# Performance work log

Hardware: AMD Instinct MI355X
Metric: run time of the kernel (lower is better)

## Reference

```python
import jax, jax.numpy as jnp
import numpy as np

B, L, N, D = 4096, 50, 50, 128
STD = 0.1


def setup_inputs() -> dict:
    key = jax.random.key(0)
    ks = jax.random.split(key, 6)
    seq_idx = jax.random.randint(ks[0], (B, L), 0, N, dtype=jnp.int32)
    mask = jnp.ones((B, L), dtype=jnp.int32)
    node_vectors = jax.random.normal(ks[1], (B, N, D), dtype=jnp.float32)
    u = lambda k, shp: jax.random.uniform(k, shp, jnp.float32, -STD, STD)
    return {
        "sequence_of_indexes": seq_idx,
        "mask": mask,
        "node_vectors": node_vectors,
        "batch_size": B,
        "W_last": u(ks[2], (D, D)),      # dense_last_item kernel (no bias)
        "W_seq": u(ks[3], (D, D)),       # dense_sequence_items kernel
        "b_seq": jnp.zeros((D,), jnp.float32),  # dense_sequence_items bias
        "W_alpha": u(ks[4], (D, 1)),     # dense_alpha kernel (no bias)
    }


def reference(sequence_of_indexes, mask, node_vectors, batch_size,
              W_last, W_seq, b_seq, W_alpha):
    maskf = mask.astype(jnp.float32)                          # [B, L]
    seq_len = jnp.sum(maskf, axis=1).astype(jnp.int32)        # [B]
    rows = jnp.arange(batch_size)
    # last item index per session, then gather its node vector
    last_idx = sequence_of_indexes[rows, seq_len - 1]         # [B]
    v_n = node_vectors[rows, last_idx]                        # [B, D]
    # per-batch embedding lookup: node_vectors[b, seq_idx[b]]
    v_i = jnp.take_along_axis(node_vectors, sequence_of_indexes[..., None], axis=1)  # [B, L, D]
    vn_proj = (v_n @ W_last)[:, None, :]                      # [B, 1, D]
    vi_proj = v_i @ W_seq + b_seq                             # [B, L, D]
    alpha = jax.nn.sigmoid(vn_proj + vi_proj) @ W_alpha       # [B, L, 1]
    alpha = alpha * maskf[..., None]
    session_graph = jnp.sum(alpha * v_i, axis=1)              # [B, D]
    return v_n, session_graph
```

## Files before the change

kernel.cpp:

```cpp
#include <hip/hip_runtime.h>
#include <math.h>

#define BB 4096
#define LL 50
#define NN 50
#define DD 128
#define STR 136

typedef short bf16x8 __attribute__((ext_vector_type(8)));
typedef float f32x4  __attribute__((ext_vector_type(4)));

static __device__ inline unsigned short f32_to_bf16_rne(float f) {
    unsigned int u = __float_as_uint(f);
    u += 0x7FFFu + ((u >> 16) & 1u);
    return (unsigned short)(u >> 16);
}
static __device__ inline float bf16_to_f32(unsigned short h) {
    return __uint_as_float(((unsigned int)h) << 16);
}

__global__ void prep_w(const float* __restrict__ W_seq,
                       const float* __restrict__ W_last,
                       unsigned short* __restrict__ ws)
{
    int t = blockIdx.x * blockDim.x + threadIdx.x;
    int lane = t & 63;
    int nt   = (t >> 6) & 7;
    int kk   = t >> 9;
    const float* W = (kk < 4) ? W_seq : W_last;
    int kb = (kk & 3) * 32 + (lane >> 4) * 8;
    int n  = nt * 16 + (lane & 15);
    unsigned short* dst = ws + (size_t)t * 8;
    #pragma unroll
    for (int j = 0; j < 8; ++j)
        dst[j] = f32_to_bf16_rne(W[(kb + j) * DD + n]);
}

__global__ __launch_bounds__(256, 3) void sess_attn(
    const int*   __restrict__ seq_idx,
    const int*   __restrict__ mask,
    const float* __restrict__ nodes,
    const float* __restrict__ b_seq,
    const float* __restrict__ W_alpha,
    const unsigned short* __restrict__ wfrag,
    float*       __restrict__ out)
{
    const int b    = blockIdx.x;
    const int tid  = threadIdx.x;
    const int lane = tid & 63;
    const int wave = tid >> 6;
    const int col  = lane & 15;
    const int quad = lane >> 4;

    __shared__ __align__(16) unsigned short s_nbf[64][STR];
    __shared__ float s_alpha[64];
    __shared__ float s_cntf[64];
    __shared__ int   s_last;

    const float4* nb4 = (const float4*)(nodes + (size_t)b * (NN * DD));
    float4 v[7];
    #pragma unroll
    for (int j = 0; j < 6; ++j) v[j] = nb4[tid + j * 256];
    if (tid < 64) v[6] = nb4[tid + 1536];

    const bf16x8* wsf = (const bf16x8*)wfrag;
    bf16x8 bfS[8], bfL[8];
    #pragma unroll
    for (int kk = 0; kk < 4; ++kk)
        #pragma unroll
        for (int j = 0; j < 2; ++j) {
            bfS[kk * 2 + j] = wsf[(size_t)(((kk    ) * 8 + wave * 2 + j) * 64 + lane)];
            bfL[kk * 2 + j] = wsf[(size_t)(((kk + 4) * 8 + wave * 2 + j) * 64 + lane)];
        }

    int pm = 0, pi = 0;
    if (tid < 64) {
        pm = (tid < LL) ? mask[b * LL + tid]    : 0;
        pi = (tid < LL) ? seq_idx[b * LL + tid] : 0;
    }

    float bb_r[2], wa_r[2];
    #pragma unroll
    for (int j = 0; j < 2; ++j) {
        int n = (wave * 2 + j) * 16 + col;
        bb_r[j] = b_seq[n];
        wa_r[j] = W_alpha[n];
    }

    if (tid < 64) { s_alpha[tid] = 0.f; s_cntf[tid] = 0.f; }

    #pragma unroll
    for (int j = 0; j < 6; ++j) {
        int idx = tid + j * 256;
        int r = idx >> 5, c = (idx & 31) * 4;
        ushort4 h;
        h.x = f32_to_bf16_rne(v[j].x);
        h.y = f32_to_bf16_rne(v[j].y);
        h.z = f32_to_bf16_rne(v[j].z);
        h.w = f32_to_bf16_rne(v[j].w);
        *(ushort4*)&s_nbf[r][c] = h;
    }
    if (tid < 64) {
        int idx = tid + 1536;
        int r = idx >> 5, c = (idx & 31) * 4;
        ushort4 h;
        h.x = f32_to_bf16_rne(v[6].x);
        h.y = f32_to_bf16_rne(v[6].y);
        h.z = f32_to_bf16_rne(v[6].z);
        h.w = f32_to_bf16_rne(v[6].w);
        *(ushort4*)&s_nbf[r][c] = h;
    }

    if (tid < 64) {
        int mm = pm;
        mm += __shfl_xor(mm, 1);  mm += __shfl_xor(mm, 2);
        mm += __shfl_xor(mm, 4);  mm += __shfl_xor(mm, 8);
        mm += __shfl_xor(mm, 16); mm += __shfl_xor(mm, 32);
        int j = mm - 1;
        if (j < 0) j += LL;
        int li = __shfl(pi, j);
        if (tid == 0) s_last = li;
        if (tid < LL && pm) atomicAdd(&s_cntf[pi], (float)pm);
    }
    __syncthreads();

    const int last = s_last;

    if (tid < DD)
        out[(size_t)b * DD + tid] = nodes[(size_t)b * (NN * DD) + last * DD + tid];

    f32x4 acc[4][2];
    #pragma unroll
    for (int m = 0; m < 4; ++m)
        #pragma unroll
        for (int j = 0; j < 2; ++j)
            acc[m][j] = (f32x4){0.f, 0.f, 0.f, 0.f};
    f32x4 accV[2];
    #pragma unroll
    for (int j = 0; j < 2; ++j)
        accV[j] = (f32x4){bb_r[j], bb_r[j], bb_r[j], bb_r[j]};

    #pragma unroll
    for (int kk = 0; kk < 4; ++kk) {
        bf16x8 a[4];
        #pragma unroll
        for (int m = 0; m < 4; ++m)
            a[m] = *(const bf16x8*)&s_nbf[m * 16 + col][kk * 32 + quad * 8];
        bf16x8 av = *(const bf16x8*)&s_nbf[last][kk * 32 + quad * 8];
        #pragma unroll
        for (int j = 0; j < 2; ++j) {
            #pragma unroll
            for (int m = 0; m < 4; ++m)
                acc[m][j] = __builtin_amdgcn_mfma_f32_16x16x32_bf16(
                    a[m], bfS[kk * 2 + j], acc[m][j], 0, 0, 0);
            accV[j] = __builtin_amdgcn_mfma_f32_16x16x32_bf16(
                av, bfL[kk * 2 + j], accV[j], 0, 0, 0);
        }
    }

    #pragma unroll
    for (int m = 0; m < 4; ++m) {
        float pr[4] = {0.f, 0.f, 0.f, 0.f};
        #pragma unroll
        for (int j = 0; j < 2; ++j) {
            float wa = wa_r[j];
            #pragma unroll
            for (int r = 0; r < 4; ++r) {
                float x = acc[m][j][r] + accV[j][r];
                float sig = 1.f / (1.f + __expf(-x));
                pr[r] = fmaf(sig, wa, pr[r]);
            }
        }
        #pragma unroll
        for (int r = 0; r < 4; ++r) {
            float vv = pr[r];
            vv += __shfl_xor(vv, 1);
            vv += __shfl_xor(vv, 2);
            vv += __shfl_xor(vv, 4);
            vv += __shfl_xor(vv, 8);
            int row = m * 16 + quad * 4 + r;
            if (col == 0 && row < NN) atomicAdd(&s_alpha[row], vv);
        }
    }
    __syncthreads();

    if (tid < DD) {
        float acc2 = 0.f;
        #pragma unroll 10
        for (int n = 0; n < NN; ++n)
            acc2 = fmaf(s_cntf[n] * s_alpha[n], bf16_to_f32(s_nbf[n][tid]), acc2);
        out[(size_t)BB * DD + (size_t)b * DD + tid] = acc2;
    }
}

extern "C" void kernel_launch(void* const* d_in, const int* in_sizes, int n_in,
                              void* d_out, int out_size, void* d_ws, size_t ws_size,
                              hipStream_t stream) {
    const int*   seq     = (const int*)  d_in[0];
    const int*   mask    = (const int*)  d_in[1];
    const float* nodes   = (const float*)d_in[2];
    const float* W_last  = (const float*)d_in[4];
    const float* W_seq   = (const float*)d_in[5];
    const float* b_seq   = (const float*)d_in[6];
    const float* W_alpha = (const float*)d_in[7];
    float*       out     = (float*)      d_out;

    unsigned short* wsf = (unsigned short*)d_ws;

    prep_w<<<16, 256, 0, stream>>>(W_seq, W_last, wsf);
    sess_attn<<<BB, 256, 0, stream>>>(seq, mask, nodes, b_seq, W_alpha, wsf, out);
}
```

Before: 177.3 us.

## Raise occupancy by deferring last-item weight loads and splitting MFMA phases

Launch bounds go from 3 to 4 blocks per SIMD/CU. To fit that, register pressure drops: the last-item weight fragments are loaded after the barrier, and the v_n projection runs after the sequence projection instead of being interleaved with it. The fp32-to-bf16 conversion now uses packed bf16x2 intrinsics. The v_n output is read back from the bf16 shared tile instead of a global fp32 reload, which saves a global read but rounds that output to bf16 precision.

```diff
diff --git a/kernel.cpp b/kernel.cpp
--- a/kernel.cpp
+++ b/kernel.cpp
@@ -1,4 +1,5 @@
 #include <hip/hip_runtime.h>
+#include <hip/hip_bf16.h>
 #include <math.h>
 
 #define BB 4096
@@ -17,6 +18,12 @@
 }
 static __device__ inline float bf16_to_f32(unsigned short h) {
     return __uint_as_float(((unsigned int)h) << 16);
+}
+static __device__ inline unsigned int pack_bf16x2(float x, float y) {
+    __hip_bfloat162 h = __float22bfloat162_rn(make_float2(x, y));
+    union { __hip_bfloat162 h2; unsigned int u; } c;
+    c.h2 = h;
+    return c.u;
 }
 
 __global__ void prep_w(const float* __restrict__ W_seq,
@@ -36,7 +43,7 @@
         dst[j] = f32_to_bf16_rne(W[(kb + j) * DD + n]);
 }
 
-__global__ __launch_bounds__(256, 3) void sess_attn(
+__global__ __launch_bounds__(256, 4) void sess_attn(
     const int*   __restrict__ seq_idx,
     const int*   __restrict__ mask,
     const float* __restrict__ nodes,
@@ -58,20 +65,19 @@
     __shared__ int   s_last;
 
     const float4* nb4 = (const float4*)(nodes + (size_t)b * (NN * DD));
-    float4 v[7];
+    float4 v[6];
     #pragma unroll
     for (int j = 0; j < 6; ++j) v[j] = nb4[tid + j * 256];
-    if (tid < 64) v[6] = nb4[tid + 1536];
+    float4 v6;
+    if (tid < 64) v6 = nb4[tid + 1536];
 
     const bf16x8* wsf = (const bf16x8*)wfrag;
-    bf16x8 bfS[8], bfL[8];
+    bf16x8 bfS[8];
     #pragma unroll
     for (int kk = 0; kk < 4; ++kk)
         #pragma unroll
-        for (int j = 0; j < 2; ++j) {
-            bfS[kk * 2 + j] = wsf[(size_t)(((kk    ) * 8 + wave * 2 + j) * 64 + lane)];
-            bfL[kk * 2 + j] = wsf[(size_t)(((kk + 4) * 8 + wave * 2 + j) * 64 + lane)];
-        }
+        for (int j = 0; j < 2; ++j)
+            bfS[kk * 2 + j] = wsf[(size_t)((kk * 8 + wave * 2 + j) * 64 + lane)];
 
     int pm = 0, pi = 0;
     if (tid < 64) {
@@ -93,22 +99,18 @@
     for (int j = 0; j < 6; ++j) {
         int idx = tid + j * 256;
         int r = idx >> 5, c = (idx & 31) * 4;
-        ushort4 h;
-        h.x = f32_to_bf16_rne(v[j].x);
-        h.y = f32_to_bf16_rne(v[j].y);
-        h.z = f32_to_bf16_rne(v[j].z);
-        h.w = f32_to_bf16_rne(v[j].w);
-        *(ushort4*)&s_nbf[r][c] = h;
+        uint2 hh;
+        hh.x = pack_bf16x2(v[j].x, v[j].y);
+        hh.y = pack_bf16x2(v[j].z, v[j].w);
+        *(uint2*)&s_nbf[r][c] = hh;
     }
     if (tid < 64) {
         int idx = tid + 1536;
         int r = idx >> 5, c = (idx & 31) * 4;
-        ushort4 h;
-        h.x = f32_to_bf16_rne(v[6].x);
-        h.y = f32_to_bf16_rne(v[6].y);
-        h.z = f32_to_bf16_rne(v[6].z);
-        h.w = f32_to_bf16_rne(v[6].w);
-        *(ushort4*)&s_nbf[r][c] = h;
+        uint2 hh;
+        hh.x = pack_bf16x2(v6.x, v6.y);
+        hh.y = pack_bf16x2(v6.z, v6.w);
+        *(uint2*)&s_nbf[r][c] = hh;
     }
 
     if (tid < 64) {
@@ -126,8 +128,12 @@
 
     const int last = s_last;
 
-    if (tid < DD)
-        out[(size_t)b * DD + tid] = nodes[(size_t)b * (NN * DD) + last * DD + tid];
+    bf16x8 bfL[8];
+    #pragma unroll
+    for (int kk = 0; kk < 4; ++kk)
+        #pragma unroll
+        for (int j = 0; j < 2; ++j)
+            bfL[kk * 2 + j] = wsf[(size_t)(((kk + 4) * 8 + wave * 2 + j) * 64 + lane)];
 
     f32x4 acc[4][2];
     #pragma unroll
@@ -135,10 +141,6 @@
         #pragma unroll
         for (int j = 0; j < 2; ++j)
             acc[m][j] = (f32x4){0.f, 0.f, 0.f, 0.f};
-    f32x4 accV[2];
-    #pragma unroll
-    for (int j = 0; j < 2; ++j)
-        accV[j] = (f32x4){bb_r[j], bb_r[j], bb_r[j], bb_r[j]};
 
     #pragma unroll
     for (int kk = 0; kk < 4; ++kk) {
@@ -146,16 +148,25 @@
         #pragma unroll
         for (int m = 0; m < 4; ++m)
             a[m] = *(const bf16x8*)&s_nbf[m * 16 + col][kk * 32 + quad * 8];
-        bf16x8 av = *(const bf16x8*)&s_nbf[last][kk * 32 + quad * 8];
-        #pragma unroll
-        for (int j = 0; j < 2; ++j) {
+        #pragma unroll
+        for (int j = 0; j < 2; ++j)
             #pragma unroll
             for (int m = 0; m < 4; ++m)
                 acc[m][j] = __builtin_amdgcn_mfma_f32_16x16x32_bf16(
                     a[m], bfS[kk * 2 + j], acc[m][j], 0, 0, 0);
+    }
+
+    f32x4 accV[2];
+    #pragma unroll
+    for (int j = 0; j < 2; ++j)
+        accV[j] = (f32x4){bb_r[j], bb_r[j], bb_r[j], bb_r[j]};
+    #pragma unroll
+    for (int kk = 0; kk < 4; ++kk) {
+        bf16x8 av = *(const bf16x8*)&s_nbf[last][kk * 32 + quad * 8];
+        #pragma unroll
+        for (int j = 0; j < 2; ++j)
             accV[j] = __builtin_amdgcn_mfma_f32_16x16x32_bf16(
                 av, bfL[kk * 2 + j], accV[j], 0, 0, 0);
-        }
     }
 
     #pragma unroll
@@ -190,6 +201,7 @@
         for (int n = 0; n < NN; ++n)
             acc2 = fmaf(s_cntf[n] * s_alpha[n], bf16_to_f32(s_nbf[n][tid]), acc2);
         out[(size_t)BB * DD + (size_t)b * DD + tid] = acc2;
+        out[(size_t)b * DD + tid] = bf16_to_f32(s_nbf[last][tid]);
     }
 }
 
```

Result: slower. 189.4 us (+6.8%).
